# Kernel tuning notes

Hardware: AMD Instinct MI355X
Metric: run time of the kernel (lower is better)

Reference implementation:

```python
import jax, jax.numpy as jnp
import numpy as np

B = 16384      # batch
CNUM = 2048    # codebook entries
K = 8          # topk
D = 10         # emb_dim
M = 50         # meta_dim
UID = 1000000
IID = 1000000
TAU = 10.0


def setup_inputs() -> dict:
    key = jax.random.key(0)
    ks = jax.random.split(key, 14)
    uid_col = jax.random.randint(ks[0], (B, 1), 0, UID, dtype=jnp.int64)
    iid_col = jax.random.randint(ks[1], (B, 1), 0, IID + 1, dtype=jnp.int64)
    x = jnp.concatenate([uid_col, iid_col], axis=1)
    return {
        "x": x,
        "gumbel_u_src": jax.random.uniform(ks[2], (B, CNUM), dtype=jnp.float32),
        "gumbel_u_tgt": jax.random.uniform(ks[3], (B, CNUM), dtype=jnp.float32),
        "src_uid_table": jax.random.normal(ks[4], (UID, D), dtype=jnp.float32),
        "tgt_uid_table": jax.random.normal(ks[5], (UID, D), dtype=jnp.float32),
        "tgt_iid_table": jax.random.normal(ks[6], (IID + 1, D), dtype=jnp.float32),
        "C": jax.random.normal(ks[7], (CNUM, M), dtype=jnp.float32) * 0.01,
        "w1": jax.random.normal(ks[8], (D, M), dtype=jnp.float32) * 0.01,
        "w2": jax.random.normal(ks[9], (M, D), dtype=jnp.float32) * 0.01,
        "mw1": jax.random.normal(ks[10], (D + M, 50), dtype=jnp.float32) * 0.1,
        "mb1": jnp.zeros((50,), dtype=jnp.float32),
        "mw2": jax.random.normal(ks[11], (50, D * D), dtype=jnp.float32) * 0.1,
        "mb2": jnp.zeros((D * D,), dtype=jnp.float32),
    }


def _gumbel_route(u_emb, C, w1, u_noise):
    # u_emb: [B, D] -> logits s_u: [B, CNUM]
    s = jnp.einsum('bm,cm->bc', u_emb @ w1, C)
    g = -jnp.log(-jnp.log(u_noise + 1e-20) + 1e-20)  # gumbel noise
    gw = jax.nn.softmax((s + g) / TAU, axis=-1)       # F.gumbel_softmax, hard=False
    tw, ti = jax.lax.top_k(gw, K)                     # [B, K]
    c_u = C[ti]                                       # [B, K, M] codebook gather
    return tw, ti, c_u


def reference(x, gumbel_u_src, gumbel_u_tgt, src_uid_table, tgt_uid_table,
              tgt_iid_table, C, w1, w2, mw1, mb1, mw2, mb2):
    # ---- stage == 'test_meta' ----
    # target-side interest embedding ('test_interst' path)
    tuid = tgt_uid_table[x[:, 0]]                      # [B, D]
    tw_t, _, c_t = _gumbel_route(tuid, C, w1, gumbel_u_tgt)
    tuid_ins = ((c_t * tw_t[..., None]).sum(axis=1)) @ w2   # [B, D]
    # source-side routing ('test_meta' path of InterstEmbedding)
    uid = src_uid_table[x[:, 0]]                       # [B, D]
    tw_s, _, c_s = _gumbel_route(uid, C, w1, gumbel_u_src)
    src_fea = jnp.broadcast_to(uid[:, None, :], (uid.shape[0], K, D))  # [B, K, D]
    inp = jnp.concatenate([c_s, src_fea], axis=-1)     # [B, K, M+D] = [B, K, 60]
    h = jax.nn.relu(inp @ mw1 + mb1)                   # [B, K, 50]
    mapping = (h @ mw2 + mb2).reshape(-1, K, D, D)     # per-sample hypernet weights
    src_emb = jnp.einsum('bkd,bkde->bke', src_fea, mapping)  # [B, K, D]
    pre_emb = (src_emb * tw_s[..., None]).sum(axis=1)  # [B, D]
    fin_emb = tuid_ins + pre_emb                       # [B, D]
    iid_emb = tgt_iid_table[x[:, 1]]                   # [B, D]
    return jnp.sum(fin_emb * iid_emb, axis=-1)         # [B]
```

## Files before the change

### kernel.cpp

```cpp
#include <hip/hip_runtime.h>
#include <hip/hip_bf16.h>


#define BROWS 16384
#define CNUM  2048
#define KSEL  8
#define DIMD  10
#define MDIM  50
#define RPB   16
#define RTPB  32
#define CH    128
#define NCH   (CNUM/CH)
#define TAUI  0.1f
#define T12   12

#define OFF_C    0
#define OFF_P16  4096
#define OFF_PF   5120
#define OFF_L    6784
#define OFF_TS   11008
#define OFF_T12  11040
#define OFF_T12L 11424
#define OFF_TW   11808
#define OFF_TI   12064
#define OFF_UD   12320
#define SMEM_W   12512

typedef float    f32x4 __attribute__((ext_vector_type(4)));
typedef _Float16 half8 __attribute__((ext_vector_type(8)));
typedef float    flt2  __attribute__((ext_vector_type(2)));
typedef unsigned int uint_t;

__device__ __forceinline__ uint_t pkrtz(float a, float b) {
    auto h = __builtin_amdgcn_cvt_pkrtz(a, b);
    union { decltype(h) v; uint_t u; } c; c.v = h; return c.u;
}
__device__ __forceinline__ float gnoise(float u) {
    return -__logf(-__logf(u + 1e-20f) + 1e-20f);
}

__global__ __launch_bounds__(256, 3)
void mf_fused(const int* __restrict__ x32,
              const float* __restrict__ gsrc,
              const float* __restrict__ gtgt,
              const float* __restrict__ suid,
              const float* __restrict__ tuid,
              const float* __restrict__ tiid,
              const float* __restrict__ Cm,
              const float* __restrict__ w1,
              const float* __restrict__ w2,
              const float* __restrict__ mw1,
              const float* __restrict__ mb1,
              const float* __restrict__ mw2,
              const float* __restrict__ mb2,
              float* __restrict__ out)
{
    __shared__ __align__(16) float smem[SMEM_W];
    __shared__ int sFlag;
    uint_t* W   = (uint_t*)smem;
    float*  sPf = smem + OFF_PF;
    float*  sL  = smem + OFF_L;
    uint_t* T12u = (uint_t*)(smem + OFF_T12);

    const int tid  = threadIdx.x;
    const int row0 = blockIdx.x * RPB;

    if (tid == 0) sFlag = 1;
    __syncthreads();
    if (tid < 128) { if (x32[2*tid+1] != 0) atomicAnd(&sFlag, 0); }
    __syncthreads();
    const int is64 = sFlag;

    for (int t = tid; t < RTPB*MDIM; t += 256) {
        const int rt = t / MDIM, mm = t - rt*MDIM;
        const int r = row0 + (rt >> 1);
        const int uidx = is64 ? x32[4*r] : x32[2*r];
        const float* tab = (rt & 1) ? suid : tuid;
        float v = 0.f;
        #pragma unroll
        for (int d = 0; d < DIMD; ++d) v += tab[uidx*DIMD + d] * w1[d*MDIM + mm];
        sPf[rt*52 + mm] = v;
    }
    __syncthreads();

    if (tid < 64) {
        const int rt = tid >> 1, hh = tid & 1;
        #pragma unroll
        for (int jj = 0; jj < 8; ++jj) {
            const int col0 = hh*32 + jj*4;
            float e0=0.f, e1=0.f, e2=0.f, e3=0.f;
            if (col0 < MDIM) {
                e0 = sPf[rt*52 + col0]; e1 = sPf[rt*52 + col0 + 1];
                if (col0 + 2 < MDIM) { e2 = sPf[rt*52 + col0 + 2]; e3 = sPf[rt*52 + col0 + 3]; }
            }
            const int wi = (OFF_P16 + rt*32 + hh*16 + jj*2) ^ ((rt & 7) << 2);
            *(uint2*)&W[wi] = make_uint2(pkrtz(e0, e1), pkrtz(e2, e3));
        }
    }

    const int srr = tid >> 1, shh = tid & 1;
    auto stageC = [&](int c0) {
        const float* crow = Cm + (c0 + srr) * MDIM;
        #pragma unroll
        for (int jj = 0; jj < 8; ++jj) {
            const int col0 = shh*32 + jj*4;
            float e0=0.f, e1=0.f, e2=0.f, e3=0.f;
            if (col0 < MDIM) {
                flt2 a = *(const flt2*)(crow + col0); e0 = a.x; e1 = a.y;
                if (col0 + 2 < MDIM) { flt2 b = *(const flt2*)(crow + col0 + 2); e2 = b.x; e3 = b.y; }
            }
            const int wi = (OFF_C + srr*32 + shh*16 + jj*2) ^ ((srr & 7) << 2);
            *(uint2*)&W[wi] = make_uint2(pkrtz(e0, e1), pkrtz(e2, e3));
        }
    };

    const int lane = tid & 63, wv = tid >> 6;
    const int lr = lane & 15, lk = lane >> 4;
    const int mt = wv & 1, nh = wv >> 1;
    const int rtA = mt*16 + lr;
    const int aw0 = (OFF_P16 + rtA*32 + 0  + lk*4) ^ ((rtA & 7) << 2);
    const int aw1 = (OFF_P16 + rtA*32 + 16 + lk*4) ^ ((rtA & 7) << 2);

    const int rtB = tid >> 3, li = tid & 7;

    float ts0 = 0.f, ts1 = 0.f;
    float q0=-3.4e38f,q1=-3.4e38f,q2=-3.4e38f,q3=-3.4e38f,
          q4=-3.4e38f,q5=-3.4e38f,q6=-3.4e38f,q7=-3.4e38f;

    stageC(0);
    __syncthreads();
    const half8 a0 = *(const half8*)&W[aw0];
    const half8 a1 = *(const half8*)&W[aw1];

    for (int ch = 0; ch < NCH; ++ch) {
        const int c0 = ch * CH;

        #pragma unroll
        for (int nt = 0; nt < 4; ++nt) {
            const int lc  = nh*64 + nt*16 + lr;
            const int bs0 = (OFF_C + lc*32 + 0  + lk*4) ^ ((lc & 7) << 2);
            const int bs1 = (OFF_C + lc*32 + 16 + lk*4) ^ ((lc & 7) << 2);
            const half8 b0 = *(const half8*)&W[bs0];
            const half8 b1 = *(const half8*)&W[bs1];
            f32x4 acc = {0.f, 0.f, 0.f, 0.f};
            acc = __builtin_amdgcn_mfma_f32_16x16x32_f16(a0, b0, acc, 0, 0, 0);
            acc = __builtin_amdgcn_mfma_f32_16x16x32_f16(a1, b1, acc, 0, 0, 0);
            #pragma unroll
            for (int r4 = 0; r4 < 4; ++r4) {
                const int rtl = mt*16 + lk*4 + r4;
                const int r = row0 + (rtl >> 1);
                const float u = ((r4 & 1) ? gsrc : gtgt)[(size_t)r*CNUM + c0 + lc];
                sL[rtl*132 + lc] = (acc[r4] + gnoise(u)) * TAUI;
            }
        }
        __syncthreads();

        if (ch + 1 < NCH) stageC((ch + 1) * CH);

        {
            f32x4 vv[4];
            #pragma unroll
            for (int j4 = 0; j4 < 4; ++j4)
                vv[j4] = *(const f32x4*)(sL + rtB*132 + li*16 + j4*4);
            #pragma unroll
            for (int j4 = 0; j4 < 4; ++j4) {
                #pragma unroll
                for (int e = 0; e < 4; ++e) {
                    const float l = vv[j4][e];
                    if (e & 1) ts1 += __expf(l); else ts0 += __expf(l);
                    const uint_t gc = (uint_t)(c0 + li*16 + j4*4 + e);
                    const float xs = __uint_as_float((__float_as_uint(l) & 0xFFFFF800u) | gc);
                    q0 = fmaxf(q0, fminf(q1, xs));
                    q1 = fmaxf(q1, fminf(q2, xs));
                    q2 = fmaxf(q2, fminf(q3, xs));
                    q3 = fmaxf(q3, fminf(q4, xs));
                    q4 = fmaxf(q4, fminf(q5, xs));
                    q5 = fmaxf(q5, fminf(q6, xs));
                    q6 = fmaxf(q6, fminf(q7, xs));
                    q7 = fmaxf(q7, xs);
                }
            }
        }
        __syncthreads();
    }

    {
        float ts = ts0 + ts1;
        ts += __shfl_xor(ts, 1, 8); ts += __shfl_xor(ts, 2, 8); ts += __shfl_xor(ts, 4, 8);
        if (li == 0) smem[OFF_TS + rtB] = ts;
        #pragma unroll
        for (int k = 0; k < T12; ++k) {
            float gm = q7;
            gm = fmaxf(gm, __shfl_xor(gm, 1, 8));
            gm = fmaxf(gm, __shfl_xor(gm, 2, 8));
            gm = fmaxf(gm, __shfl_xor(gm, 4, 8));
            if (q7 == gm) { q7=q6; q6=q5; q5=q4; q4=q3; q3=q2; q2=q1; q1=q0; q0=-3.4e38f; }
            if (li == (k & 7)) T12u[rtB*T12 + k] = __float_as_uint(gm);
        }
    }
    __syncthreads();

    for (int T = tid; T < RTPB*T12; T += 256) {
        const int rt = T / T12, j = T - rt*T12;
        const int idx = (int)(T12u[rt*T12 + j] & 2047u);
        const float* pf = sPf + rt*52;
        const float* cr = Cm + idx*MDIM;
        float s = 0.f;
        #pragma unroll
        for (int k2 = 0; k2 < 25; ++k2) {
            flt2 c = *(const flt2*)(cr + k2*2);
            s += pf[2*k2] * c.x + pf[2*k2+1] * c.y;
        }
        const int r = row0 + (rt >> 1);
        const float u = ((rt & 1) ? gsrc : gtgt)[(size_t)r*CNUM + idx];
        smem[OFF_T12L + rt*T12 + j] = (s + gnoise(u)) * TAUI;
    }
    __syncthreads();

    if (tid < RTPB) {
        const int rt = tid;
        const float inv = 1.0f / smem[OFF_TS + rt];
        float lv[T12]; int iv[T12];
        #pragma unroll
        for (int j = 0; j < T12; ++j) {
            lv[j] = smem[OFF_T12L + rt*T12 + j];
            iv[j] = (int)(T12u[rt*T12 + j] & 2047u);
        }
        uint_t used = 0;
        #pragma unroll
        for (int k = 0; k < KSEL; ++k) {
            float bl = -3.4e38f; int bi = 1 << 30; int bj = 0;
            #pragma unroll
            for (int j = 0; j < T12; ++j) {
                const bool ok = !((used >> j) & 1);
                if (ok && (lv[j] > bl || (lv[j] == bl && iv[j] < bi))) { bl = lv[j]; bi = iv[j]; bj = j; }
            }
            used |= 1u << bj;
            smem[OFF_TW + rt*KSEL + k] = __expf(bl) * inv;
            ((int*)smem)[OFF_TI + rt*KSEL + k] = bi;
        }
    }
    __syncthreads();

    float* sH    = smem;
    float* sQ    = smem + 832;
    float* sUd   = smem + OFF_UD;
    float* sTopW = smem + OFF_TW;
    int*   sTopI = (int*)smem + OFF_TI;

    const int g = tid >> 4, lg = tid & 15;
    const int row = row0 + g;
    const int rt_t = g*2, rt_s = g*2 + 1;
    const int uidx = is64 ? x32[4*row]     : x32[2*row];
    const int iidx = is64 ? x32[4*row + 2] : x32[2*row + 1];

    if (lg < DIMD) sUd[g*12 + lg] = suid[uidx*DIMD + lg];
    __syncthreads();

    for (int t = lg; t < MDIM*DIMD; t += 16) {
        const int j = t / DIMD, e = t - j*DIMD;
        float q = 0.f;
        #pragma unroll
        for (int d = 0; d < DIMD; ++d) q += sUd[g*12 + d] * mw2[j*(DIMD*DIMD) + d*DIMD + e];
        sQ[g*500 + t] = q;
    }
    for (int mm = lg; mm < MDIM; mm += 16) {
        float v = 0.f;
        #pragma unroll
        for (int k = 0; k < KSEL; ++k)
            v += sTopW[rt_t*KSEL + k] * Cm[sTopI[rt_t*KSEL + k]*MDIM + mm];
        sH[g*52 + mm] = v;
    }
    __syncthreads();

    float acc_e = 0.f, be = 0.f;
    if (lg < DIMD) {
        for (int m2 = 0; m2 < MDIM; ++m2) acc_e += sH[g*52 + m2] * w2[m2*DIMD + lg];
        #pragma unroll
        for (int d = 0; d < DIMD; ++d) be += sUd[g*12 + d] * mb2[d*DIMD + lg];
    }
    __syncthreads();

    for (int k = 0; k < KSEL; ++k) {
        const int   ik = sTopI[rt_s*KSEL + k];
        const float tw = sTopW[rt_s*KSEL + k];
        for (int j = lg; j < MDIM; j += 16) {
            float h = mb1[j];
            const float* crow = Cm + ik*MDIM;
            for (int t2 = 0; t2 < MDIM; ++t2) h += crow[t2] * mw1[t2*MDIM + j];
            #pragma unroll
            for (int d = 0; d < DIMD; ++d) h += sUd[g*12 + d] * mw1[(MDIM + d)*MDIM + j];
            sH[g*52 + j] = fmaxf(h, 0.f);
        }
        __syncthreads();
        if (lg < DIMD) {
            float se = be;
            for (int j = 0; j < MDIM; ++j) se += sH[g*52 + j] * sQ[g*500 + j*DIMD + lg];
            acc_e += tw * se;
        }
        __syncthreads();
    }

    float o = 0.f;
    if (lg < DIMD) o = acc_e * tiid[iidx*DIMD + lg];
    #pragma unroll
    for (int k = 8; k >= 1; k >>= 1) o += __shfl_xor(o, k, 16);
    if (lg == 0) out[row] = o;
}

extern "C" void kernel_launch(void* const* d_in, const int* in_sizes, int n_in,
                              void* d_out, int out_size, void* d_ws, size_t ws_size,
                              hipStream_t stream) {
    (void)in_sizes; (void)n_in; (void)out_size; (void)d_ws; (void)ws_size;
    const int*   x32  = (const int*)d_in[0];
    const float* gsrc = (const float*)d_in[1];
    const float* gtgt = (const float*)d_in[2];
    const float* suid = (const float*)d_in[3];
    const float* tuid = (const float*)d_in[4];
    const float* tiid = (const float*)d_in[5];
    const float* Cm   = (const float*)d_in[6];
    const float* w1   = (const float*)d_in[7];
    const float* w2   = (const float*)d_in[8];
    const float* mw1  = (const float*)d_in[9];
    const float* mb1  = (const float*)d_in[10];
    const float* mw2  = (const float*)d_in[11];
    const float* mb2  = (const float*)d_in[12];
    hipLaunchKernelGGL(mf_fused, dim3(BROWS/RPB), dim3(256), 0, stream,
                       x32, gsrc, gtgt, suid, tuid, tiid, Cm, w1, w2, mw1, mb1, mw2, mb2,
                       (float*)d_out);
}
```

Baseline: 300.4 us.

## Double-buffer fp16 codebook via pre-pass and fuse top-k scan into MFMA epilogue

Adds a small pre-kernel that converts the codebook to packed fp16 in workspace, so each block streams it with wide loads into a double-buffered LDS tile. The next chunk is loaded into registers while the current chunk's MFMAs run. The logits staging buffer and its extra barrier pass are removed: softmax sums and the per-thread top-8 run directly on MFMA accumulators, with the noise read as float4 vectors. Because each thread now covers a different slice of columns, the candidate pool is widened from 12 to 24 per row before exact rescoring, at the cost of more rescoring work and an extra launch.

```diff
diff --git a/kernel.cpp b/kernel.cpp
--- a/kernel.cpp
+++ b/kernel.cpp
@@ -12,33 +12,41 @@
 #define CH    128
 #define NCH   (CNUM/CH)
 #define TAUI  0.1f
-#define T12   12
-
-#define OFF_C    0
-#define OFF_P16  4096
-#define OFF_PF   5120
-#define OFF_L    6784
-#define OFF_TS   11008
-#define OFF_T12  11040
-#define OFF_T12L 11424
-#define OFF_TW   11808
-#define OFF_TI   12064
-#define OFF_UD   12320
-#define SMEM_W   12512
+#define T24   24
+
+#define OFF_C0   0
+#define OFF_C1   4096
+#define OFF_PF   8192
+#define OFF_T24  9856
+#define OFF_T24L 10624
+#define OFF_TS   11392
+#define OFF_TW   11456
+#define OFF_TI   11712
+#define OFF_UD   11968
+#define SMEM_W   12160
 
 typedef float    f32x4 __attribute__((ext_vector_type(4)));
 typedef _Float16 half8 __attribute__((ext_vector_type(8)));
 typedef float    flt2  __attribute__((ext_vector_type(2)));
-typedef unsigned int uint_t;
-
-__device__ __forceinline__ uint_t pkrtz(float a, float b) {
+typedef unsigned int u32;
+
+__device__ __forceinline__ u32 pkrtz(float a, float b) {
     auto h = __builtin_amdgcn_cvt_pkrtz(a, b);
-    union { decltype(h) v; uint_t u; } c; c.v = h; return c.u;
+    union { decltype(h) v; u32 u; } c; c.v = h; return c.u;
 }
 __device__ __forceinline__ float gnoise(float u) {
     return -__logf(-__logf(u + 1e-20f) + 1e-20f);
 }
 
+__global__ void cvtC(const float* __restrict__ Cm, u32* __restrict__ C16) {
+    const int j = blockIdx.x * 256 + threadIdx.x;
+    const int cand = j >> 5, w = j & 31, k = 2 * w;
+    const float a = (k < MDIM)     ? Cm[cand*MDIM + k]     : 0.f;
+    const float b = (k + 1 < MDIM) ? Cm[cand*MDIM + k + 1] : 0.f;
+    C16[j] = pkrtz(a, b);
+}
+
+template<bool PRE>
 __global__ __launch_bounds__(256, 3)
 void mf_fused(const int* __restrict__ x32,
               const float* __restrict__ gsrc,
@@ -53,14 +61,15 @@
               const float* __restrict__ mb1,
               const float* __restrict__ mw2,
               const float* __restrict__ mb2,
+              const u32* __restrict__ C16,
               float* __restrict__ out)
 {
     __shared__ __align__(16) float smem[SMEM_W];
     __shared__ int sFlag;
-    uint_t* W   = (uint_t*)smem;
-    float*  sPf = smem + OFF_PF;
-    float*  sL  = smem + OFF_L;
-    uint_t* T12u = (uint_t*)(smem + OFF_T12);
+    u32*   W    = (u32*)smem;
+    float* sPf  = smem + OFF_PF;
+    u32*   T24u = (u32*)(smem + OFF_T24);
+    float* T24l = smem + OFF_T24L;
 
     const int tid  = threadIdx.x;
     const int row0 = blockIdx.x * RPB;
@@ -71,139 +80,133 @@
     __syncthreads();
     const int is64 = sFlag;
 
-    for (int t = tid; t < RTPB*MDIM; t += 256) {
-        const int rt = t / MDIM, mm = t - rt*MDIM;
-        const int r = row0 + (rt >> 1);
-        const int uidx = is64 ? x32[4*r] : x32[2*r];
-        const float* tab = (rt & 1) ? suid : tuid;
+    for (int t = tid; t < RTPB*52; t += 256) {
+        const int rt = t / 52, mm = t - rt*52;
         float v = 0.f;
-        #pragma unroll
-        for (int d = 0; d < DIMD; ++d) v += tab[uidx*DIMD + d] * w1[d*MDIM + mm];
-        sPf[rt*52 + mm] = v;
-    }
-    __syncthreads();
-
-    if (tid < 64) {
-        const int rt = tid >> 1, hh = tid & 1;
-        #pragma unroll
-        for (int jj = 0; jj < 8; ++jj) {
-            const int col0 = hh*32 + jj*4;
-            float e0=0.f, e1=0.f, e2=0.f, e3=0.f;
-            if (col0 < MDIM) {
-                e0 = sPf[rt*52 + col0]; e1 = sPf[rt*52 + col0 + 1];
-                if (col0 + 2 < MDIM) { e2 = sPf[rt*52 + col0 + 2]; e3 = sPf[rt*52 + col0 + 3]; }
+        if (mm < MDIM) {
+            const int r = row0 + (rt >> 1);
+            const int uidx = is64 ? x32[4*r] : x32[2*r];
+            const float* tab = (rt & 1) ? suid : tuid;
+            #pragma unroll
+            for (int d = 0; d < DIMD; ++d) v += tab[uidx*DIMD + d] * w1[d*MDIM + mm];
+        }
+        sPf[t] = v;
+    }
+
+    u32 sw[16];
+    const int xorv = ((tid >> 3) & 7) << 2;
+    auto issue = [&](int ch) {
+        if (PRE) {
+            const uint4* src = (const uint4*)C16;
+            #pragma unroll
+            for (int i = 0; i < 4; ++i) {
+                uint4 t4 = src[ch*1024 + i*256 + tid];
+                sw[i*4+0] = t4.x; sw[i*4+1] = t4.y; sw[i*4+2] = t4.z; sw[i*4+3] = t4.w;
             }
-            const int wi = (OFF_P16 + rt*32 + hh*16 + jj*2) ^ ((rt & 7) << 2);
-            *(uint2*)&W[wi] = make_uint2(pkrtz(e0, e1), pkrtz(e2, e3));
-        }
-    }
-
-    const int srr = tid >> 1, shh = tid & 1;
-    auto stageC = [&](int c0) {
-        const float* crow = Cm + (c0 + srr) * MDIM;
-        #pragma unroll
-        for (int jj = 0; jj < 8; ++jj) {
-            const int col0 = shh*32 + jj*4;
-            float e0=0.f, e1=0.f, e2=0.f, e3=0.f;
-            if (col0 < MDIM) {
-                flt2 a = *(const flt2*)(crow + col0); e0 = a.x; e1 = a.y;
-                if (col0 + 2 < MDIM) { flt2 b = *(const flt2*)(crow + col0 + 2); e2 = b.x; e3 = b.y; }
-            }
-            const int wi = (OFF_C + srr*32 + shh*16 + jj*2) ^ ((srr & 7) << 2);
-            *(uint2*)&W[wi] = make_uint2(pkrtz(e0, e1), pkrtz(e2, e3));
+        } else {
+            #pragma unroll
+            for (int i = 0; i < 4; ++i)
+                #pragma unroll
+                for (int w2i = 0; w2i < 4; ++w2i) {
+                    const int cand = ch*CH + (tid >> 3) + i*32;
+                    const int widx = (tid*4 + w2i) & 31, k = 2*widx;
+                    const float a = (k < MDIM)     ? Cm[cand*MDIM + k]     : 0.f;
+                    const float b = (k + 1 < MDIM) ? Cm[cand*MDIM + k + 1] : 0.f;
+                    sw[i*4 + w2i] = pkrtz(a, b);
+                }
         }
     };
+    auto commit = [&](int buf) {
+        u32* B = W + buf*4096;
+        #pragma unroll
+        for (int i = 0; i < 4; ++i)
+            *(uint4*)&B[(tid*4 + i*1024) ^ xorv] =
+                make_uint4(sw[i*4], sw[i*4+1], sw[i*4+2], sw[i*4+3]);
+    };
+
+    issue(0); commit(0);
+    __syncthreads();
 
     const int lane = tid & 63, wv = tid >> 6;
     const int lr = lane & 15, lk = lane >> 4;
-    const int mt = wv & 1, nh = wv >> 1;
-    const int rtA = mt*16 + lr;
-    const int aw0 = (OFF_P16 + rtA*32 + 0  + lk*4) ^ ((rtA & 7) << 2);
-    const int aw1 = (OFF_P16 + rtA*32 + 16 + lk*4) ^ ((rtA & 7) << 2);
-
-    const int rtB = tid >> 3, li = tid & 7;
-
-    float ts0 = 0.f, ts1 = 0.f;
+    const int g = wv & 1, h = wv >> 1;
+    const int rt = g*16 + lr;
+    const int xorr = (lr & 7) << 2;
+    const float* up = ((lr & 1) ? gsrc : gtgt) + (size_t)(row0 + g*8 + (lr >> 1)) * CNUM;
+
+    half8 b0, b1;
+    {
+        union { u32 u[4]; half8 v; } c0, c1;
+        #pragma unroll
+        for (int jj = 0; jj < 4; ++jj) {
+            const int k0 = lk*8 + jj*2;
+            c0.u[jj] = pkrtz(sPf[rt*52 + k0], sPf[rt*52 + k0 + 1]);
+            const int k1 = 32 + lk*8 + jj*2;
+            const float e0 = (k1     < 52) ? sPf[rt*52 + k1]     : 0.f;
+            const float e1 = (k1 + 1 < 52) ? sPf[rt*52 + k1 + 1] : 0.f;
+            c1.u[jj] = pkrtz(e0, e1);
+        }
+        b0 = c0.v; b1 = c1.v;
+    }
+
+    float ts = 0.f;
     float q0=-3.4e38f,q1=-3.4e38f,q2=-3.4e38f,q3=-3.4e38f,
           q4=-3.4e38f,q5=-3.4e38f,q6=-3.4e38f,q7=-3.4e38f;
 
-    stageC(0);
-    __syncthreads();
-    const half8 a0 = *(const half8*)&W[aw0];
-    const half8 a1 = *(const half8*)&W[aw1];
-
     for (int ch = 0; ch < NCH; ++ch) {
-        const int c0 = ch * CH;
-
+        if (ch + 1 < NCH) issue(ch + 1);
+        const u32* Bf = W + (ch & 1)*4096;
         #pragma unroll
         for (int nt = 0; nt < 4; ++nt) {
-            const int lc  = nh*64 + nt*16 + lr;
-            const int bs0 = (OFF_C + lc*32 + 0  + lk*4) ^ ((lc & 7) << 2);
-            const int bs1 = (OFF_C + lc*32 + 16 + lk*4) ^ ((lc & 7) << 2);
-            const half8 b0 = *(const half8*)&W[bs0];
-            const half8 b1 = *(const half8*)&W[bs1];
+            const int cl = h*64 + nt*16;
+            const int wb = (cl + lr) * 32;
+            const half8 a0 = *(const half8*)&Bf[(wb +      lk*4) ^ xorr];
+            const half8 a1 = *(const half8*)&Bf[(wb + 16 + lk*4) ^ xorr];
             f32x4 acc = {0.f, 0.f, 0.f, 0.f};
             acc = __builtin_amdgcn_mfma_f32_16x16x32_f16(a0, b0, acc, 0, 0, 0);
             acc = __builtin_amdgcn_mfma_f32_16x16x32_f16(a1, b1, acc, 0, 0, 0);
+            const f32x4 u4 = *(const f32x4*)(up + ch*CH + cl + lk*4);
+            const int cg = ch*CH + cl + lk*4;
             #pragma unroll
             for (int r4 = 0; r4 < 4; ++r4) {
-                const int rtl = mt*16 + lk*4 + r4;
-                const int r = row0 + (rtl >> 1);
-                const float u = ((r4 & 1) ? gsrc : gtgt)[(size_t)r*CNUM + c0 + lc];
-                sL[rtl*132 + lc] = (acc[r4] + gnoise(u)) * TAUI;
+                const float l = (acc[r4] + gnoise(u4[r4])) * TAUI;
+                ts += __expf(l);
+                const float xs = __uint_as_float(
+                    (__float_as_uint(l) & 0xFFFFF800u) | (u32)(cg + r4));
+                q0 = fmaxf(q0, fminf(q1, xs));
+                q1 = fmaxf(q1, fminf(q2, xs));
+                q2 = fmaxf(q2, fminf(q3, xs));
+                q3 = fmaxf(q3, fminf(q4, xs));
+                q4 = fmaxf(q4, fminf(q5, xs));
+                q5 = fmaxf(q5, fminf(q6, xs));
+                q6 = fmaxf(q6, fminf(q7, xs));
+                q7 = fmaxf(q7, xs);
             }
         }
+        if (ch + 1 < NCH) commit((ch + 1) & 1);
         __syncthreads();
-
-        if (ch + 1 < NCH) stageC((ch + 1) * CH);
-
-        {
-            f32x4 vv[4];
-            #pragma unroll
-            for (int j4 = 0; j4 < 4; ++j4)
-                vv[j4] = *(const f32x4*)(sL + rtB*132 + li*16 + j4*4);
-            #pragma unroll
-            for (int j4 = 0; j4 < 4; ++j4) {
-                #pragma unroll
-                for (int e = 0; e < 4; ++e) {
-                    const float l = vv[j4][e];
-                    if (e & 1) ts1 += __expf(l); else ts0 += __expf(l);
-                    const uint_t gc = (uint_t)(c0 + li*16 + j4*4 + e);
-                    const float xs = __uint_as_float((__float_as_uint(l) & 0xFFFFF800u) | gc);
-                    q0 = fmaxf(q0, fminf(q1, xs));
-                    q1 = fmaxf(q1, fminf(q2, xs));
-                    q2 = fmaxf(q2, fminf(q3, xs));
-                    q3 = fmaxf(q3, fminf(q4, xs));
-                    q4 = fmaxf(q4, fminf(q5, xs));
-                    q5 = fmaxf(q5, fminf(q6, xs));
-                    q6 = fmaxf(q6, fminf(q7, xs));
-                    q7 = fmaxf(q7, xs);
-                }
+    }
+
+    {
+        float tss = ts;
+        tss += __shfl_xor(tss, 16); tss += __shfl_xor(tss, 32);
+        if (lk == 0) smem[OFF_TS + rt*2 + h] = tss;
+        #pragma unroll
+        for (int k = 0; k < 12; ++k) {
+            float gm = fmaxf(q7, __shfl_xor(q7, 16));
+            gm = fmaxf(gm, __shfl_xor(gm, 32));
+            if (q7 == gm) {
+                T24u[rt*T24 + h*12 + k] = __float_as_uint(q7);
+                q7=q6; q6=q5; q5=q4; q4=q3; q3=q2; q2=q1; q1=q0; q0=-3.4e38f;
             }
         }
-        __syncthreads();
-    }
-
-    {
-        float ts = ts0 + ts1;
-        ts += __shfl_xor(ts, 1, 8); ts += __shfl_xor(ts, 2, 8); ts += __shfl_xor(ts, 4, 8);
-        if (li == 0) smem[OFF_TS + rtB] = ts;
-        #pragma unroll
-        for (int k = 0; k < T12; ++k) {
-            float gm = q7;
-            gm = fmaxf(gm, __shfl_xor(gm, 1, 8));
-            gm = fmaxf(gm, __shfl_xor(gm, 2, 8));
-            gm = fmaxf(gm, __shfl_xor(gm, 4, 8));
-            if (q7 == gm) { q7=q6; q6=q5; q5=q4; q4=q3; q3=q2; q2=q1; q1=q0; q0=-3.4e38f; }
-            if (li == (k & 7)) T12u[rtB*T12 + k] = __float_as_uint(gm);
-        }
-    }
-    __syncthreads();
-
-    for (int T = tid; T < RTPB*T12; T += 256) {
-        const int rt = T / T12, j = T - rt*T12;
-        const int idx = (int)(T12u[rt*T12 + j] & 2047u);
-        const float* pf = sPf + rt*52;
+    }
+    __syncthreads();
+
+    for (int e = tid; e < RTPB*T24; e += 256) {
+        const int ert = e / T24;
+        const int idx = (int)(T24u[e] & 2047u);
+        const float* pf = sPf + ert*52;
         const float* cr = Cm + idx*MDIM;
         float s = 0.f;
         #pragma unroll
@@ -211,33 +214,33 @@
             flt2 c = *(const flt2*)(cr + k2*2);
             s += pf[2*k2] * c.x + pf[2*k2+1] * c.y;
         }
-        const int r = row0 + (rt >> 1);
-        const float u = ((rt & 1) ? gsrc : gtgt)[(size_t)r*CNUM + idx];
-        smem[OFF_T12L + rt*T12 + j] = (s + gnoise(u)) * TAUI;
+        const int r = row0 + (ert >> 1);
+        const float u = ((ert & 1) ? gsrc : gtgt)[(size_t)r*CNUM + idx];
+        T24l[e] = (s + gnoise(u)) * TAUI;
     }
     __syncthreads();
 
     if (tid < RTPB) {
-        const int rt = tid;
-        const float inv = 1.0f / smem[OFF_TS + rt];
-        float lv[T12]; int iv[T12];
-        #pragma unroll
-        for (int j = 0; j < T12; ++j) {
-            lv[j] = smem[OFF_T12L + rt*T12 + j];
-            iv[j] = (int)(T12u[rt*T12 + j] & 2047u);
-        }
-        uint_t used = 0;
+        const int rrt = tid;
+        const float inv = 1.0f / (smem[OFF_TS + rrt*2] + smem[OFF_TS + rrt*2 + 1]);
+        float lv[T24]; int iv[T24];
+        #pragma unroll
+        for (int j = 0; j < T24; ++j) {
+            lv[j] = T24l[rrt*T24 + j];
+            iv[j] = (int)(T24u[rrt*T24 + j] & 2047u);
+        }
+        u32 used = 0;
         #pragma unroll
         for (int k = 0; k < KSEL; ++k) {
             float bl = -3.4e38f; int bi = 1 << 30; int bj = 0;
             #pragma unroll
-            for (int j = 0; j < T12; ++j) {
+            for (int j = 0; j < T24; ++j) {
                 const bool ok = !((used >> j) & 1);
                 if (ok && (lv[j] > bl || (lv[j] == bl && iv[j] < bi))) { bl = lv[j]; bi = iv[j]; bj = j; }
             }
             used |= 1u << bj;
-            smem[OFF_TW + rt*KSEL + k] = __expf(bl) * inv;
-            ((int*)smem)[OFF_TI + rt*KSEL + k] = bi;
+            smem[OFF_TW + rrt*KSEL + k] = __expf(bl) * inv;
+            ((int*)smem)[OFF_TI + rrt*KSEL + k] = bi;
         }
     }
     __syncthreads();
@@ -248,36 +251,36 @@
     float* sTopW = smem + OFF_TW;
     int*   sTopI = (int*)smem + OFF_TI;
 
-    const int g = tid >> 4, lg = tid & 15;
-    const int row = row0 + g;
-    const int rt_t = g*2, rt_s = g*2 + 1;
+    const int gg = tid >> 4, lg = tid & 15;
+    const int row = row0 + gg;
+    const int rt_t = gg*2, rt_s = gg*2 + 1;
     const int uidx = is64 ? x32[4*row]     : x32[2*row];
     const int iidx = is64 ? x32[4*row + 2] : x32[2*row + 1];
 
-    if (lg < DIMD) sUd[g*12 + lg] = suid[uidx*DIMD + lg];
+    if (lg < DIMD) sUd[gg*12 + lg] = suid[uidx*DIMD + lg];
     __syncthreads();
 
     for (int t = lg; t < MDIM*DIMD; t += 16) {
         const int j = t / DIMD, e = t - j*DIMD;
         float q = 0.f;
         #pragma unroll
-        for (int d = 0; d < DIMD; ++d) q += sUd[g*12 + d] * mw2[j*(DIMD*DIMD) + d*DIMD + e];
-        sQ[g*500 + t] = q;
+        for (int d = 0; d < DIMD; ++d) q += sUd[gg*12 + d] * mw2[j*(DIMD*DIMD) + d*DIMD + e];
+        sQ[gg*500 + t] = q;
     }
     for (int mm = lg; mm < MDIM; mm += 16) {
         float v = 0.f;
         #pragma unroll
         for (int k = 0; k < KSEL; ++k)
             v += sTopW[rt_t*KSEL + k] * Cm[sTopI[rt_t*KSEL + k]*MDIM + mm];
-        sH[g*52 + mm] = v;
+        sH[gg*52 + mm] = v;
     }
     __syncthreads();
 
     float acc_e = 0.f, be = 0.f;
     if (lg < DIMD) {
-        for (int m2 = 0; m2 < MDIM; ++m2) acc_e += sH[g*52 + m2] * w2[m2*DIMD + lg];
-        #pragma unroll
-        for (int d = 0; d < DIMD; ++d) be += sUd[g*12 + d] * mb2[d*DIMD + lg];
+        for (int m2 = 0; m2 < MDIM; ++m2) acc_e += sH[gg*52 + m2] * w2[m2*DIMD + lg];
+        #pragma unroll
+        for (int d = 0; d < DIMD; ++d) be += sUd[gg*12 + d] * mb2[d*DIMD + lg];
     }
     __syncthreads();
 
@@ -285,17 +288,17 @@
         const int   ik = sTopI[rt_s*KSEL + k];
         const float tw = sTopW[rt_s*KSEL + k];
         for (int j = lg; j < MDIM; j += 16) {
-            float h = mb1[j];
+            float hh = mb1[j];
             const float* crow = Cm + ik*MDIM;
-            for (int t2 = 0; t2 < MDIM; ++t2) h += crow[t2] * mw1[t2*MDIM + j];
-            #pragma unroll
-            for (int d = 0; d < DIMD; ++d) h += sUd[g*12 + d] * mw1[(MDIM + d)*MDIM + j];
-            sH[g*52 + j] = fmaxf(h, 0.f);
+            for (int t2 = 0; t2 < MDIM; ++t2) hh += crow[t2] * mw1[t2*MDIM + j];
+            #pragma unroll
+            for (int d = 0; d < DIMD; ++d) hh += sUd[gg*12 + d] * mw1[(MDIM + d)*MDIM + j];
+            sH[gg*52 + j] = fmaxf(hh, 0.f);
         }
         __syncthreads();
         if (lg < DIMD) {
             float se = be;
-            for (int j = 0; j < MDIM; ++j) se += sH[g*52 + j] * sQ[g*500 + j*DIMD + lg];
+            for (int j = 0; j < MDIM; ++j) se += sH[gg*52 + j] * sQ[gg*500 + j*DIMD + lg];
             acc_e += tw * se;
         }
         __syncthreads();
@@ -311,7 +314,7 @@
 extern "C" void kernel_launch(void* const* d_in, const int* in_sizes, int n_in,
                               void* d_out, int out_size, void* d_ws, size_t ws_size,
                               hipStream_t stream) {
-    (void)in_sizes; (void)n_in; (void)out_size; (void)d_ws; (void)ws_size;
+    (void)in_sizes; (void)n_in; (void)out_size;
     const int*   x32  = (const int*)d_in[0];
     const float* gsrc = (const float*)d_in[1];
     const float* gtgt = (const float*)d_in[2];
@@ -325,7 +328,16 @@
     const float* mb1  = (const float*)d_in[10];
     const float* mw2  = (const float*)d_in[11];
     const float* mb2  = (const float*)d_in[12];
-    hipLaunchKernelGGL(mf_fused, dim3(BROWS/RPB), dim3(256), 0, stream,
-                       x32, gsrc, gtgt, suid, tuid, tiid, Cm, w1, w2, mw1, mb1, mw2, mb2,
-                       (float*)d_out);
-}
+    u32* C16 = (u32*)d_ws;
+
+    if (ws_size >= 262144) {
+        hipLaunchKernelGGL(cvtC, dim3(256), dim3(256), 0, stream, Cm, C16);
+        hipLaunchKernelGGL(mf_fused<true>, dim3(BROWS/RPB), dim3(256), 0, stream,
+                           x32, gsrc, gtgt, suid, tuid, tiid, Cm, w1, w2, mw1, mb1, mw2, mb2,
+                           C16, (float*)d_out);
+    } else {
+        hipLaunchKernelGGL(mf_fused<false>, dim3(BROWS/RPB), dim3(256), 0, stream,
+                           x32, gsrc, gtgt, suid, tuid, tiid, Cm, w1, w2, mw1, mb1, mw2, mb2,
+                           C16, (float*)d_out);
+    }
+}
```

New measurement: 290.6 us. 1.03x faster.
